# Optimization experiments

Measured on AMD Instinct MI355X. Metric: run time of the kernel, lower is better.

The kernel has to match this reference:

```python
import jax, jax.numpy as jnp
import numpy as np

K = 3          # kernel size (both dims)
PAD = 1        # padding used both for offset_mask conv and deform_conv2d
KK = K * K


def setup_inputs() -> dict:
    key = jax.random.key(0)
    k0, k1, k2, k3, k4 = jax.random.split(key, 5)
    B, C, H, W, O = 8, 64, 64, 64, 64
    input_feat = jax.random.normal(k0, (B, C, H, W), jnp.float32)
    degrad_inter = jax.random.normal(k1, (B, C, H, W), jnp.float32)
    stdv = 1.0 / np.sqrt(C * K * K)
    weight = jax.random.uniform(k2, (O, C, K, K), jnp.float32, -stdv, stdv)
    # small-magnitude offset/mask conv params -> realistic small learned offsets
    om_weight = jax.random.normal(k3, (3 * KK, 2 * C, K, K), jnp.float32) * 0.01
    om_bias = jax.random.normal(k4, (3 * KK,), jnp.float32) * 0.01
    return {"input_feat": input_feat, "degrad_inter": degrad_inter,
            "weight": weight, "om_weight": om_weight, "om_bias": om_bias}


def _conv2d(x, w, b):
    out = jax.lax.conv_general_dilated(
        x, w, window_strides=(1, 1), padding=((PAD, PAD), (PAD, PAD)),
        dimension_numbers=("NCHW", "OIHW", "NCHW"))
    return out + b[None, :, None, None]


def _deform_conv2d(x, offset, mask, weight):
    # x: (B,C,H,W); offset: (B,2*KK,H,W) with channel 2k=dy_k, 2k+1=dx_k;
    # mask: (B,KK,H,W); weight: (O,C,K,K). stride=1, padding=PAD, dilation=1.
    B, C, H, W = x.shape
    O = weight.shape[0]
    off = offset.reshape(B, KK, 2, H, W)
    dy, dx = off[:, :, 0], off[:, :, 1]                       # (B,KK,H,W)

    ky, kx = jnp.meshgrid(jnp.arange(K), jnp.arange(K), indexing="ij")
    ky = ky.reshape(KK).astype(x.dtype)
    kx = kx.reshape(KK).astype(x.dtype)
    hh = jnp.arange(H, dtype=x.dtype)
    ww = jnp.arange(W, dtype=x.dtype)
    # absolute fractional sample locations: (B,KK,H,W)
    y = hh[None, None, :, None] - PAD + ky[None, :, None, None] + dy
    xq = ww[None, None, None, :] - PAD + kx[None, :, None, None] + dx

    y0 = jnp.floor(y).astype(jnp.int32)
    x0 = jnp.floor(xq).astype(jnp.int32)
    y1, x1 = y0 + 1, x0 + 1
    wy = y - y0.astype(x.dtype)
    wx = xq - x0.astype(x.dtype)

    x_flat = x.reshape(B, C, H * W)

    def gather(yi, xi):
        valid = (yi >= 0) & (yi < H) & (xi >= 0) & (xi < W)
        idx = jnp.clip(yi, 0, H - 1) * W + jnp.clip(xi, 0, W - 1)  # (B,KK,H,W)
        vals = jax.vmap(lambda im, ix: im[:, ix])(x_flat, idx)     # (B,C,KK,H,W)
        return vals * valid[:, None].astype(x.dtype)

    wy_ = wy[:, None]  # (B,1,KK,H,W)
    wx_ = wx[:, None]
    sampled = (gather(y0, x0) * (1 - wy_) * (1 - wx_)
               + gather(y0, x1) * (1 - wy_) * wx_
               + gather(y1, x0) * wy_ * (1 - wx_)
               + gather(y1, x1) * wy_ * wx_)                       # (B,C,KK,H,W)
    sampled = sampled * mask[:, None]
    return jnp.einsum("bckhw,ock->bohw", sampled, weight.reshape(O, C, KK))


def reference(input_feat, degrad_inter, weight, om_weight, om_bias):
    concat = jnp.concatenate([input_feat, degrad_inter], axis=1)
    om = _conv2d(concat, om_weight, om_bias)                       # (B,3*KK,H,W)
    off1, off2, mask = jnp.split(om, 3, axis=1)
    offset = jnp.concatenate([off1, off2], axis=1)                 # (B,2*KK,H,W)
    mask = jax.nn.sigmoid(mask)                                    # (B,KK,H,W)
    return _deform_conv2d(input_feat, offset, mask, weight)
```

## Files before the change

kernel.cpp:

```cpp
#include <hip/hip_runtime.h>
#include <math.h>

#define WO_PK_OFF 36864
#define CATT_OFF  73728

typedef short  short8  __attribute__((ext_vector_type(8)));
typedef float  float4v __attribute__((ext_vector_type(4)));

static __device__ __forceinline__ short f2bf(float f) {
    unsigned int u = __builtin_bit_cast(unsigned int, f);
    u += 0x7FFFu + ((u >> 16) & 1u);
    return (short)(u >> 16);
}
static __device__ __forceinline__ float bf2f(unsigned short u) {
    return __builtin_bit_cast(float, (unsigned int)u << 16);
}

__global__ __launch_bounds__(256) void prep_w(
    const float* __restrict__ weight, const float* __restrict__ om_weight,
    short* __restrict__ wd_pk, short* __restrict__ wo_pk)
{
    int idx = blockIdx.x * 256 + threadIdx.x;
    if (idx < 36864) {
        int j = idx & 7, o = (idx >> 3) & 63, lq = (idx >> 9) & 3, ks = idx >> 11;
        int t = ks >> 1, c = (ks & 1) * 32 + lq * 8 + j;
        wd_pk[idx] = f2bf(weight[(o * 64 + c) * 9 + t]);
    } else {
        int e = idx - 36864;
        int j = e & 7, oc = (e >> 3) & 31, lq = (e >> 8) & 3, ks2 = e >> 10;
        int quarter = ks2 / 9, t = ks2 - quarter * 9;
        int cg = quarter * 32 + lq * 8 + j;
        wo_pk[e] = (oc < 27) ? f2bf(om_weight[(oc * 128 + cg) * 9 + t])
                             : (short)0;
    }
}

__global__ __launch_bounds__(256) void transpose_kernel(
    const float* __restrict__ feat, const float* __restrict__ deg,
    unsigned short* __restrict__ catT)
{
    __shared__ unsigned short T[64 * 136];
    const int b = blockIdx.x >> 6, h = blockIdx.x & 63;
    const int tid = threadIdx.x;
    const int lane = tid & 63, wv = tid >> 6;
#pragma unroll
    for (int cc = 0; cc < 32; cc++) {
        int c = wv * 32 + cc;
        const float* src = (c < 64)
            ? (feat + (size_t)(b * 64 + c) * 4096)
            : (deg  + (size_t)(b * 64 + (c - 64)) * 4096);
        T[lane * 136 + c] = (unsigned short)f2bf(src[h * 64 + lane]);
    }
    __syncthreads();
    const int px = tid >> 2, seg = tid & 3;
    unsigned short* dst = catT + (size_t)(b * 4096 + h * 64 + px) * 128 + seg * 32;
#pragma unroll
    for (int j = 0; j < 4; j++)
        *(uint4*)(dst + j * 8) = *(const uint4*)&T[px * 136 + seg * 32 + j * 8];
}

__global__ __launch_bounds__(256) void fused_kernel(
    const unsigned short* __restrict__ catT, const short* __restrict__ wd_pk,
    const short* __restrict__ wo_pk, const float* __restrict__ om_bias,
    float* __restrict__ out)
{
    __shared__ float T[4 * 16 * 36];
    const int tid = threadIdx.x;
    const int lane = tid & 63, wv = tid >> 6;
    const int l16 = lane & 15, lq = lane >> 4;
    const int gw = blockIdx.x * 4 + wv;
    const int b = gw >> 8, tile = gw & 255;
    const int h = tile >> 2, w0 = (tile & 3) << 4;
    const int pxx = w0 + l16;
    const unsigned short* cb = catT + (size_t)b * 4096 * 128;

    float4v oacc0 = {0.f, 0.f, 0.f, 0.f};
    float4v oacc1 = {0.f, 0.f, 0.f, 0.f};
    const short8 zf = {0, 0, 0, 0, 0, 0, 0, 0};
#pragma unroll
    for (int quarter = 0; quarter < 4; quarter++) {
#pragma unroll
        for (int t = 0; t < 9; t++) {
            const int ky = t / 3, kx = t - ky * 3;
            const int yy = h - 1 + ky;
            if (yy >= 0 && yy <= 63) {
                int xx = pxx - 1 + kx;
                bool okx = (xx >= 0) & (xx <= 63);
                int xc = min(max(xx, 0), 63);
                short8 bfr = *(const short8*)(cb + (yy * 64 + xc) * 128
                                                 + quarter * 32 + lq * 8);
                bfr = okx ? bfr : zf;
                const short8* Ap = (const short8*)(wo_pk
                    + (size_t)((quarter * 9 + t) * 4 + lq) * 256);
                oacc0 = __builtin_amdgcn_mfma_f32_16x16x32_bf16(
                    Ap[l16], bfr, oacc0, 0, 0, 0);
                oacc1 = __builtin_amdgcn_mfma_f32_16x16x32_bf16(
                    Ap[16 + l16], bfr, oacc1, 0, 0, 0);
            }
        }
    }

    float* Tw = T + wv * 576;
#pragma unroll
    for (int r = 0; r < 4; r++) {
        Tw[l16 * 36 + lq * 4 + r]      = oacc0[r];
        Tw[l16 * 36 + 16 + lq * 4 + r] = oacc1[r];
    }
    __syncthreads();
    float omv[28];
#pragma unroll
    for (int jj = 0; jj < 7; jj++)
        *(float4v*)&omv[jj * 4] = *(const float4v*)&Tw[l16 * 36 + jj * 4];
#pragma unroll
    for (int j = 0; j < 27; j++) omv[j] += om_bias[j];

    float4v acc[4];
#pragma unroll
    for (int mt = 0; mt < 4; mt++) acc[mt] = (float4v){0.f, 0.f, 0.f, 0.f};
#pragma unroll
    for (int t = 0; t < 9; t++) {
        const int ky = t / 3, kx = t - ky * 3;
        float dy = omv[2 * t], dx = omv[2 * t + 1];
        float mm = 1.f / (1.f + __expf(-omv[18 + t]));
        float yf = (float)(h - 1 + ky) + dy;
        float xf = (float)(pxx - 1 + kx) + dx;
        float fy = floorf(yf), fx = floorf(xf);
        int y0 = (int)fy, x0 = (int)fx;
        float wy = yf - fy, wx = xf - fx;
        bool vy0 = (y0 >= 0) & (y0 < 64);
        bool vy1 = (y0 >= -1) & (y0 < 63);
        bool vx0 = (x0 >= 0) & (x0 < 64);
        bool vx1 = (x0 >= -1) & (x0 < 63);
        float a0 = (1.f - wy) * mm, a1 = wy * mm;
        float W00 = a0 * (1.f - wx) * (float)(vy0 & vx0);
        float W01 = a0 * wx         * (float)(vy0 & vx1);
        float W10 = a1 * (1.f - wx) * (float)(vy1 & vx0);
        float W11 = a1 * wx         * (float)(vy1 & vx1);
        int iy0 = min(max(y0, 0), 63),     ix0 = min(max(x0, 0), 63);
        int iy1 = min(max(y0 + 1, 0), 63), ix1 = min(max(x0 + 1, 0), 63);
        int O00 = (iy0 * 64 + ix0) * 128, O01 = (iy0 * 64 + ix1) * 128;
        int O10 = (iy1 * 64 + ix0) * 128, O11 = (iy1 * 64 + ix1) * 128;
#pragma unroll
        for (int qh = 0; qh < 2; qh++) {
            const int cho = qh * 32 + lq * 8;
            short8 c00 = *(const short8*)(cb + O00 + cho);
            short8 c01 = *(const short8*)(cb + O01 + cho);
            short8 c10 = *(const short8*)(cb + O10 + cho);
            short8 c11 = *(const short8*)(cb + O11 + cho);
            short8 bfr;
#pragma unroll
            for (int j = 0; j < 8; j++) {
                float s = W00 * bf2f((unsigned short)c00[j])
                        + W01 * bf2f((unsigned short)c01[j])
                        + W10 * bf2f((unsigned short)c10[j])
                        + W11 * bf2f((unsigned short)c11[j]);
                bfr[j] = f2bf(s);
            }
            const short8* Dp = (const short8*)(wd_pk
                + (size_t)((t * 2 + qh) * 4 + lq) * 512);
            acc[0] = __builtin_amdgcn_mfma_f32_16x16x32_bf16(
                Dp[l16], bfr, acc[0], 0, 0, 0);
            acc[1] = __builtin_amdgcn_mfma_f32_16x16x32_bf16(
                Dp[16 + l16], bfr, acc[1], 0, 0, 0);
            acc[2] = __builtin_amdgcn_mfma_f32_16x16x32_bf16(
                Dp[32 + l16], bfr, acc[2], 0, 0, 0);
            acc[3] = __builtin_amdgcn_mfma_f32_16x16x32_bf16(
                Dp[48 + l16], bfr, acc[3], 0, 0, 0);
        }
    }

    float* ob = out + (size_t)(b * 64) * 4096 + h * 64 + w0 + l16;
#pragma unroll
    for (int mt = 0; mt < 4; mt++)
#pragma unroll
        for (int r = 0; r < 4; r++)
            ob[(mt * 16 + lq * 4 + r) * 4096] = acc[mt][r];
}

extern "C" void kernel_launch(void* const* d_in, const int* in_sizes, int n_in,
                              void* d_out, int out_size, void* d_ws, size_t ws_size,
                              hipStream_t stream)
{
    const float* feat      = (const float*)d_in[0];
    const float* deg       = (const float*)d_in[1];
    const float* weight    = (const float*)d_in[2];
    const float* om_weight = (const float*)d_in[3];
    const float* om_bias   = (const float*)d_in[4];
    float* out = (float*)d_out;
    short* wss = (short*)d_ws;
    unsigned short* catT = (unsigned short*)(wss + CATT_OFF);

    hipLaunchKernelGGL(prep_w,           dim3(288), dim3(256), 0, stream,
                       weight, om_weight, wss, wss + WO_PK_OFF);
    hipLaunchKernelGGL(transpose_kernel, dim3(512), dim3(256), 0, stream,
                       feat, deg, catT);
    hipLaunchKernelGGL(fused_kernel,     dim3(512), dim3(256), 0, stream,
                       catT, wss, wss + WO_PK_OFF, om_bias, out);
}
```

Before: 113.2 us.

## Merge weight prep into transpose kernel and software-pipeline gathers in fused kernel

Folds the weight-packing kernel into the transpose kernel as extra blocks, so one launch is removed. In the fused kernel, the offset-conv loop and the deformable sampling loop are flattened and double-buffered: the next step's global loads are issued before the current MFMAs run. Bilinear weights and offsets for all nine taps are precomputed into arrays, and launch_bounds(256,2) is added. The prefetching raises register pressure, and the flattened offset-conv loop now issues loads for out-of-range rows as well.

```diff
diff --git a/kernel.cpp b/kernel.cpp
--- a/kernel.cpp
+++ b/kernel.cpp
@@ -16,55 +16,57 @@
     return __builtin_bit_cast(float, (unsigned int)u << 16);
 }
 
-__global__ __launch_bounds__(256) void prep_w(
+__global__ __launch_bounds__(256) void prep_transpose(
+    const float* __restrict__ feat, const float* __restrict__ deg,
     const float* __restrict__ weight, const float* __restrict__ om_weight,
+    unsigned short* __restrict__ catT,
     short* __restrict__ wd_pk, short* __restrict__ wo_pk)
 {
-    int idx = blockIdx.x * 256 + threadIdx.x;
-    if (idx < 36864) {
-        int j = idx & 7, o = (idx >> 3) & 63, lq = (idx >> 9) & 3, ks = idx >> 11;
-        int t = ks >> 1, c = (ks & 1) * 32 + lq * 8 + j;
-        wd_pk[idx] = f2bf(weight[(o * 64 + c) * 9 + t]);
+    __shared__ unsigned short T[64 * 136];
+    const int tid = threadIdx.x;
+    if (blockIdx.x < 512) {
+        const int b = blockIdx.x >> 6, h = blockIdx.x & 63;
+        const int lane = tid & 63, wv = tid >> 6;
+#pragma unroll
+        for (int cc = 0; cc < 32; cc++) {
+            int c = wv * 32 + cc;
+            const float* src = (c < 64)
+                ? (feat + (size_t)(b * 64 + c) * 4096)
+                : (deg  + (size_t)(b * 64 + (c - 64)) * 4096);
+            T[lane * 136 + c] = (unsigned short)f2bf(src[h * 64 + lane]);
+        }
+        __syncthreads();
+        const int px = tid >> 2, seg = tid & 3;
+        unsigned short* dst =
+            catT + (size_t)(b * 4096 + h * 64 + px) * 128 + seg * 32;
+#pragma unroll
+        for (int j = 0; j < 4; j++)
+            *(uint4*)(dst + j * 8) = *(const uint4*)&T[px * 136 + seg * 32 + j * 8];
     } else {
-        int e = idx - 36864;
-        int j = e & 7, oc = (e >> 3) & 31, lq = (e >> 8) & 3, ks2 = e >> 10;
-        int quarter = ks2 / 9, t = ks2 - quarter * 9;
-        int cg = quarter * 32 + lq * 8 + j;
-        wo_pk[e] = (oc < 27) ? f2bf(om_weight[(oc * 128 + cg) * 9 + t])
-                             : (short)0;
-    }
-}
-
-__global__ __launch_bounds__(256) void transpose_kernel(
-    const float* __restrict__ feat, const float* __restrict__ deg,
-    unsigned short* __restrict__ catT)
-{
-    __shared__ unsigned short T[64 * 136];
-    const int b = blockIdx.x >> 6, h = blockIdx.x & 63;
-    const int tid = threadIdx.x;
-    const int lane = tid & 63, wv = tid >> 6;
-#pragma unroll
-    for (int cc = 0; cc < 32; cc++) {
-        int c = wv * 32 + cc;
-        const float* src = (c < 64)
-            ? (feat + (size_t)(b * 64 + c) * 4096)
-            : (deg  + (size_t)(b * 64 + (c - 64)) * 4096);
-        T[lane * 136 + c] = (unsigned short)f2bf(src[h * 64 + lane]);
-    }
-    __syncthreads();
-    const int px = tid >> 2, seg = tid & 3;
-    unsigned short* dst = catT + (size_t)(b * 4096 + h * 64 + px) * 128 + seg * 32;
-#pragma unroll
-    for (int j = 0; j < 4; j++)
-        *(uint4*)(dst + j * 8) = *(const uint4*)&T[px * 136 + seg * 32 + j * 8];
-}
-
-__global__ __launch_bounds__(256) void fused_kernel(
+        int idx = (blockIdx.x - 512) * 256 + tid;
+        if (idx < 36864) {
+            int j = idx & 7, o = (idx >> 3) & 63;
+            int lq = (idx >> 9) & 3, ks = idx >> 11;
+            int t = ks >> 1, c = (ks & 1) * 32 + lq * 8 + j;
+            wd_pk[idx] = f2bf(weight[(o * 64 + c) * 9 + t]);
+        } else {
+            int e = idx - 36864;
+            int j = e & 7, oc = (e >> 3) & 31;
+            int lq = (e >> 8) & 3, ks2 = e >> 10;
+            int quarter = ks2 / 9, t = ks2 - quarter * 9;
+            int cg = quarter * 32 + lq * 8 + j;
+            wo_pk[e] = (oc < 27) ? f2bf(om_weight[(oc * 128 + cg) * 9 + t])
+                                 : (short)0;
+        }
+    }
+}
+
+__global__ __launch_bounds__(256, 2) void fused_kernel(
     const unsigned short* __restrict__ catT, const short* __restrict__ wd_pk,
     const short* __restrict__ wo_pk, const float* __restrict__ om_bias,
     float* __restrict__ out)
 {
-    __shared__ float T[4 * 16 * 36];
+    __shared__ float T[4 * 576];
     const int tid = threadIdx.x;
     const int lane = tid & 63, wv = tid >> 6;
     const int l16 = lane & 15, lq = lane >> 4;
@@ -73,31 +75,29 @@
     const int h = tile >> 2, w0 = (tile & 3) << 4;
     const int pxx = w0 + l16;
     const unsigned short* cb = catT + (size_t)b * 4096 * 128;
-
+    const short8 zf = {0, 0, 0, 0, 0, 0, 0, 0};
+
+    auto loadB1 = [&](int s) -> short8 {
+        int quarter = s / 9, t = s - quarter * 9;
+        int ky = t / 3, kx = t - ky * 3;
+        int yy = h - 1 + ky, xx = pxx - 1 + kx;
+        bool ok = (yy >= 0) & (yy <= 63) & (xx >= 0) & (xx <= 63);
+        int yc = min(max(yy, 0), 63), xc = min(max(xx, 0), 63);
+        short8 v = *(const short8*)(cb + (yc * 64 + xc) * 128
+                                       + quarter * 32 + lq * 8);
+        return ok ? v : zf;
+    };
     float4v oacc0 = {0.f, 0.f, 0.f, 0.f};
     float4v oacc1 = {0.f, 0.f, 0.f, 0.f};
-    const short8 zf = {0, 0, 0, 0, 0, 0, 0, 0};
-#pragma unroll
-    for (int quarter = 0; quarter < 4; quarter++) {
-#pragma unroll
-        for (int t = 0; t < 9; t++) {
-            const int ky = t / 3, kx = t - ky * 3;
-            const int yy = h - 1 + ky;
-            if (yy >= 0 && yy <= 63) {
-                int xx = pxx - 1 + kx;
-                bool okx = (xx >= 0) & (xx <= 63);
-                int xc = min(max(xx, 0), 63);
-                short8 bfr = *(const short8*)(cb + (yy * 64 + xc) * 128
-                                                 + quarter * 32 + lq * 8);
-                bfr = okx ? bfr : zf;
-                const short8* Ap = (const short8*)(wo_pk
-                    + (size_t)((quarter * 9 + t) * 4 + lq) * 256);
-                oacc0 = __builtin_amdgcn_mfma_f32_16x16x32_bf16(
-                    Ap[l16], bfr, oacc0, 0, 0, 0);
-                oacc1 = __builtin_amdgcn_mfma_f32_16x16x32_bf16(
-                    Ap[16 + l16], bfr, oacc1, 0, 0, 0);
-            }
-        }
+    short8 b1 = loadB1(0);
+#pragma unroll
+    for (int s = 0; s < 36; s++) {
+        short8 bn = zf;
+        if (s + 1 < 36) bn = loadB1(s + 1);
+        const short8* Ap = (const short8*)(wo_pk + (size_t)(s * 4 + lq) * 256);
+        oacc0 = __builtin_amdgcn_mfma_f32_16x16x32_bf16(Ap[l16], b1, oacc0, 0, 0, 0);
+        oacc1 = __builtin_amdgcn_mfma_f32_16x16x32_bf16(Ap[16 + l16], b1, oacc1, 0, 0, 0);
+        b1 = bn;
     }
 
     float* Tw = T + wv * 576;
@@ -114,9 +114,8 @@
 #pragma unroll
     for (int j = 0; j < 27; j++) omv[j] += om_bias[j];
 
-    float4v acc[4];
-#pragma unroll
-    for (int mt = 0; mt < 4; mt++) acc[mt] = (float4v){0.f, 0.f, 0.f, 0.f};
+    float Wb[9][4];
+    int   Ob[9][4];
 #pragma unroll
     for (int t = 0; t < 9; t++) {
         const int ky = t / 3, kx = t - ky * 3;
@@ -132,41 +131,49 @@
         bool vx0 = (x0 >= 0) & (x0 < 64);
         bool vx1 = (x0 >= -1) & (x0 < 63);
         float a0 = (1.f - wy) * mm, a1 = wy * mm;
-        float W00 = a0 * (1.f - wx) * (float)(vy0 & vx0);
-        float W01 = a0 * wx         * (float)(vy0 & vx1);
-        float W10 = a1 * (1.f - wx) * (float)(vy1 & vx0);
-        float W11 = a1 * wx         * (float)(vy1 & vx1);
+        Wb[t][0] = a0 * (1.f - wx) * (float)(vy0 & vx0);
+        Wb[t][1] = a0 * wx         * (float)(vy0 & vx1);
+        Wb[t][2] = a1 * (1.f - wx) * (float)(vy1 & vx0);
+        Wb[t][3] = a1 * wx         * (float)(vy1 & vx1);
         int iy0 = min(max(y0, 0), 63),     ix0 = min(max(x0, 0), 63);
         int iy1 = min(max(y0 + 1, 0), 63), ix1 = min(max(x0 + 1, 0), 63);
-        int O00 = (iy0 * 64 + ix0) * 128, O01 = (iy0 * 64 + ix1) * 128;
-        int O10 = (iy1 * 64 + ix0) * 128, O11 = (iy1 * 64 + ix1) * 128;
-#pragma unroll
-        for (int qh = 0; qh < 2; qh++) {
-            const int cho = qh * 32 + lq * 8;
-            short8 c00 = *(const short8*)(cb + O00 + cho);
-            short8 c01 = *(const short8*)(cb + O01 + cho);
-            short8 c10 = *(const short8*)(cb + O10 + cho);
-            short8 c11 = *(const short8*)(cb + O11 + cho);
-            short8 bfr;
-#pragma unroll
-            for (int j = 0; j < 8; j++) {
-                float s = W00 * bf2f((unsigned short)c00[j])
-                        + W01 * bf2f((unsigned short)c01[j])
-                        + W10 * bf2f((unsigned short)c10[j])
-                        + W11 * bf2f((unsigned short)c11[j]);
-                bfr[j] = f2bf(s);
-            }
-            const short8* Dp = (const short8*)(wd_pk
-                + (size_t)((t * 2 + qh) * 4 + lq) * 512);
-            acc[0] = __builtin_amdgcn_mfma_f32_16x16x32_bf16(
-                Dp[l16], bfr, acc[0], 0, 0, 0);
-            acc[1] = __builtin_amdgcn_mfma_f32_16x16x32_bf16(
-                Dp[16 + l16], bfr, acc[1], 0, 0, 0);
-            acc[2] = __builtin_amdgcn_mfma_f32_16x16x32_bf16(
-                Dp[32 + l16], bfr, acc[2], 0, 0, 0);
-            acc[3] = __builtin_amdgcn_mfma_f32_16x16x32_bf16(
-                Dp[48 + l16], bfr, acc[3], 0, 0, 0);
+        Ob[t][0] = (iy0 * 64 + ix0) * 128;  Ob[t][1] = (iy0 * 64 + ix1) * 128;
+        Ob[t][2] = (iy1 * 64 + ix0) * 128;  Ob[t][3] = (iy1 * 64 + ix1) * 128;
+    }
+
+    float4v acc[4];
+#pragma unroll
+    for (int mt = 0; mt < 4; mt++) acc[mt] = (float4v){0.f, 0.f, 0.f, 0.f};
+
+    auto loadC = [&](int s, short8* c) {
+        int t = s >> 1, qh = s & 1;
+        int cho = qh * 32 + lq * 8;
+#pragma unroll
+        for (int r = 0; r < 4; r++)
+            c[r] = *(const short8*)(cb + Ob[t][r] + cho);
+    };
+    short8 cur[4], nxt[4];
+    loadC(0, cur);
+#pragma unroll
+    for (int s = 0; s < 18; s++) {
+        if (s + 1 < 18) loadC(s + 1, nxt);
+        const int t = s >> 1;
+        short8 bfr;
+#pragma unroll
+        for (int j = 0; j < 8; j++) {
+            float v = Wb[t][0] * bf2f((unsigned short)cur[0][j])
+                    + Wb[t][1] * bf2f((unsigned short)cur[1][j])
+                    + Wb[t][2] * bf2f((unsigned short)cur[2][j])
+                    + Wb[t][3] * bf2f((unsigned short)cur[3][j]);
+            bfr[j] = f2bf(v);
         }
+        const short8* Dp = (const short8*)(wd_pk + (size_t)(s * 4 + lq) * 512);
+        acc[0] = __builtin_amdgcn_mfma_f32_16x16x32_bf16(Dp[l16],      bfr, acc[0], 0, 0, 0);
+        acc[1] = __builtin_amdgcn_mfma_f32_16x16x32_bf16(Dp[16 + l16], bfr, acc[1], 0, 0, 0);
+        acc[2] = __builtin_amdgcn_mfma_f32_16x16x32_bf16(Dp[32 + l16], bfr, acc[2], 0, 0, 0);
+        acc[3] = __builtin_amdgcn_mfma_f32_16x16x32_bf16(Dp[48 + l16], bfr, acc[3], 0, 0, 0);
+#pragma unroll
+        for (int r = 0; r < 4; r++) cur[r] = nxt[r];
     }
 
     float* ob = out + (size_t)(b * 64) * 4096 + h * 64 + w0 + l16;
@@ -190,10 +197,9 @@
     short* wss = (short*)d_ws;
     unsigned short* catT = (unsigned short*)(wss + CATT_OFF);
 
-    hipLaunchKernelGGL(prep_w,           dim3(288), dim3(256), 0, stream,
-                       weight, om_weight, wss, wss + WO_PK_OFF);
-    hipLaunchKernelGGL(transpose_kernel, dim3(512), dim3(256), 0, stream,
-                       feat, deg, catT);
-    hipLaunchKernelGGL(fused_kernel,     dim3(512), dim3(256), 0, stream,
+    hipLaunchKernelGGL(prep_transpose, dim3(800), dim3(256), 0, stream,
+                       feat, deg, weight, om_weight, catT,
+                       wss, wss + WO_PK_OFF);
+    hipLaunchKernelGGL(fused_kernel,   dim3(512), dim3(256), 0, stream,
                        catT, wss, wss + WO_PK_OFF, om_bias, out);
 }
```

Result: slower. 119.8 us (+5.8%).
